# Optimization experiments

Measured on AMD Instinct MI355X. Metric: run time of the kernel, lower is better.

The kernel has to match this reference:

```python
import jax, jax.numpy as jnp
import numpy as np

N, P, D = 8, 4096, 3


def _chamfer_one_direction(x, y, x_lengths, y_lengths):
    # x: (N,P1,D), y: (N,P2,D); squared-L2 k=1 NN of each x point in y (norm=2 in knn_points)
    P1 = x.shape[1]
    P2 = y.shape[1]
    x2 = jnp.sum(x * x, axis=-1)  # (N,P1)
    y2 = jnp.sum(y * y, axis=-1)  # (N,P2)
    d2 = x2[:, :, None] + y2[:, None, :] - 2.0 * jnp.einsum('npd,nqd->npq', x, y)  # (N,P1,P2)
    # mask padded y points out of the NN search
    y_mask = jnp.arange(P2)[None, :] >= y_lengths[:, None]  # (N,P2) True = padded
    d2 = jnp.where(y_mask[:, None, :], jnp.inf, d2)
    cham = jnp.min(d2, axis=2)  # (N,P1) dist to nearest valid y
    # zero out padded x points
    x_mask = jnp.arange(P1)[None, :] >= x_lengths[:, None]  # (N,P1)
    cham = jnp.where(x_mask, 0.0, cham)
    # point_reduction='mean'
    per_cloud = jnp.sum(cham, axis=1) / jnp.maximum(x_lengths, 1).astype(x.dtype)  # (N,)
    # batch_reduction='mean' (no weights -> divide by N)
    return jnp.sum(per_cloud) / x.shape[0]


def setup_inputs() -> dict:
    key = jax.random.key(0)
    k1, k2, k3, k4 = jax.random.split(key, 4)
    x = jax.random.normal(k1, (N, P, D), dtype=jnp.float32)
    y = jax.random.normal(k2, (N, P, D), dtype=jnp.float32)
    x_lengths = jax.random.randint(k3, (N,), P // 2, P + 1)
    y_lengths = jax.random.randint(k4, (N,), P // 2, P + 1)
    return {"x": x, "y": y, "x_lengths": x_lengths, "y_lengths": y_lengths}


def reference(x, y, x_lengths, y_lengths):
    cham_x = _chamfer_one_direction(x, y, x_lengths, y_lengths)
    cham_y = _chamfer_one_direction(y, x, y_lengths, x_lengths)
    return cham_x + cham_y
```

## Files before the change

kernel.cpp:

```cpp
#include <hip/hip_runtime.h>
#include <hip/hip_bf16.h>
#include <math.h>

constexpr int NB  = 8;
constexpr int PP  = 4096;

constexpr int TPB = 256;
constexpr int XPT = 4;
constexpr int XCH = TPB * XPT;
constexpr int NXC = PP / XCH;
constexpr int NYC = 32;
constexpr int YCH = PP / NYC;
constexpr int GRIDA = 2 * NB * NXC * NYC;

constexpr int NSEG = 16;
constexpr int SEGP = PP / NSEG;
constexpr int NPART = 2 * NB * NSEG;

__global__ __launch_bounds__(TPB, 4) void nn_partial(
    const float* __restrict__ x, const float* __restrict__ y,
    const int* __restrict__ xlen, const int* __restrict__ ylen,
    float* __restrict__ ws)
{
    __shared__ float4 sy[YCH];

    const int bid = (int)blockIdx.x;
    const int yc  = bid & (NYC - 1);
    const int xc  = (bid >> 5) & (NXC - 1);
    const int n   = (bid >> 7) & (NB - 1);
    const int dir = bid >> 10;

    const float* __restrict__ xs = dir ? y : x;
    const float* __restrict__ ys = dir ? x : y;
    const int yl = (dir ? xlen : ylen)[n];
    const int ql = (dir ? ylen : xlen)[n];

    const float* __restrict__ yb = ys + (size_t)n * PP * 3;
    if ((int)threadIdx.x < YCH) {
        const int p   = (int)threadIdx.x;
        const int idx = yc + NYC * p;
        float y0 = yb[idx * 3 + 0];
        float y1 = yb[idx * 3 + 1];
        float y2 = yb[idx * 3 + 2];
        sy[p] = make_float4(-2.f * y0, -2.f * y1, -2.f * y2,
                            fmaf(y0, y0, fmaf(y1, y1, y2 * y2)));
    }

    const int wave  = (int)threadIdx.x >> 6;
    const int lane  = (int)threadIdx.x & 63;
    const int wbase = xc * XCH + wave * (XPT * 64);

    float px0[XPT], px1[XPT], px2[XPT], a[XPT], emin[XPT];
    const float* __restrict__ xb = xs + (size_t)n * PP * 3;
#pragma unroll
    for (int k = 0; k < XPT; ++k) {
        const int xi = wbase + k * 64 + lane;
        px0[k] = xb[xi * 3 + 0];
        px1[k] = xb[xi * 3 + 1];
        px2[k] = xb[xi * 3 + 2];
        a[k]   = fmaf(px0[k], px0[k], fmaf(px1[k], px1[k], px2[k] * px2[k]));
        emin[k] = INFINITY;
    }
    __syncthreads();

    int jend = (yl - yc + NYC - 1) >> 5;
    if (jend > YCH) jend = YCH;

    if (ql > wbase && jend > 0) {
        const int j2 = jend & ~1;
#pragma unroll 2
        for (int j = 0; j < j2; j += 2) {
            const float4 u = sy[j];
            const float4 v = sy[j + 1];
#pragma unroll
            for (int k = 0; k < XPT; ++k) {
                float e1 = fmaf(px0[k], u.x, fmaf(px1[k], u.y, fmaf(px2[k], u.z, u.w)));
                float e2 = fmaf(px0[k], v.x, fmaf(px1[k], v.y, fmaf(px2[k], v.z, v.w)));
                emin[k] = fminf(emin[k], fminf(e1, e2));
            }
        }
        if (jend & 1) {
            const float4 u = sy[jend - 1];
#pragma unroll
            for (int k = 0; k < XPT; ++k) {
                float e1 = fmaf(px0[k], u.x, fmaf(px1[k], u.y, fmaf(px2[k], u.z, u.w)));
                emin[k] = fminf(emin[k], e1);
            }
        }
    }

    float* __restrict__ w = ws + ((size_t)(dir * NB + n) * NYC + yc) * PP;
#pragma unroll
    for (int k = 0; k < XPT; ++k) {
        w[wbase + k * 64 + lane] = a[k] + emin[k];
    }
}

__global__ __launch_bounds__(256) void reduce_cloud(
    const float* __restrict__ ws,
    const int* __restrict__ xlen, const int* __restrict__ ylen,
    float* __restrict__ partial)
{
    const int b   = blockIdx.x;
    const int seg = b & (NSEG - 1);
    const int c   = b >> 4;
    const int dir = c >> 3;
    const int n   = c & (NB - 1);
    const int xl  = (dir ? ylen : xlen)[n];

    const float* __restrict__ w = ws + (size_t)c * NYC * PP;
    const int i = seg * SEGP + (int)threadIdx.x;

    float m = w[i];
#pragma unroll
    for (int ch = 1; ch < NYC; ++ch) m = fminf(m, w[(size_t)ch * PP + i]);
    float sum = (i < xl) ? m : 0.f;

#pragma unroll
    for (int off = 32; off > 0; off >>= 1) sum += __shfl_xor(sum, off);
    __shared__ float ls[4];
    const int lane = (int)threadIdx.x & 63;
    const int wv   = (int)threadIdx.x >> 6;
    if (lane == 0) ls[wv] = sum;
    __syncthreads();
    if (threadIdx.x == 0) {
        float tot = ls[0] + ls[1] + ls[2] + ls[3];
        int d = xl > 1 ? xl : 1;
        partial[b] = tot / (float)d / (float)NB;
    }
}

__global__ __launch_bounds__(256) void final_sum(
    const float* __restrict__ partial, float* __restrict__ out)
{
    float v = partial[threadIdx.x];
#pragma unroll
    for (int off = 32; off > 0; off >>= 1) v += __shfl_xor(v, off);
    __shared__ float ls[4];
    const int lane = (int)threadIdx.x & 63;
    const int wv   = (int)threadIdx.x >> 6;
    if (lane == 0) ls[wv] = v;
    __syncthreads();
    if (threadIdx.x == 0) out[0] = ls[0] + ls[1] + ls[2] + ls[3];
}

__global__ __launch_bounds__(TPB) void chamfer_atomic(
    const float* __restrict__ x, const float* __restrict__ y,
    const int* __restrict__ xlen, const int* __restrict__ ylen,
    float* __restrict__ out)
{
    __shared__ float4 sy[YCH];

    int bid = blockIdx.x;
    const int xc  = bid & (NXC - 1); bid >>= 2;
    const int n   = bid & (NB - 1);  bid >>= 3;
    const int dir = bid;

    const float* __restrict__ xs = dir ? y : x;
    const float* __restrict__ ys = dir ? x : y;
    const int yl = (dir ? xlen : ylen)[n];
    const int xl = (dir ? ylen : xlen)[n];

    float m0[XPT], m1[XPT], m2[XPT], a[XPT], emin[XPT];
    const int xi0 = xc * XCH + (int)threadIdx.x;
    const float* __restrict__ xb = xs + (size_t)n * PP * 3;
#pragma unroll
    for (int k = 0; k < XPT; ++k) {
        int xi = xi0 + k * TPB;
        float x0 = xb[xi * 3 + 0];
        float x1 = xb[xi * 3 + 1];
        float x2 = xb[xi * 3 + 2];
        m0[k] = -2.f * x0; m1[k] = -2.f * x1; m2[k] = -2.f * x2;
        a[k]  = fmaf(x0, x0, fmaf(x1, x1, x2 * x2));
        emin[k] = INFINITY;
    }

    for (int yc = 0; yc < NYC; ++yc) {
        const float* __restrict__ ybase = ys + ((size_t)n * PP + (size_t)yc * YCH) * 3;
        __syncthreads();
        if ((int)threadIdx.x < YCH) {
            int p = (int)threadIdx.x;
            float y0 = ybase[p * 3 + 0];
            float y1 = ybase[p * 3 + 1];
            float y2 = ybase[p * 3 + 2];
            sy[p] = make_float4(y0, y1, y2, fmaf(y0, y0, fmaf(y1, y1, y2 * y2)));
        }
        __syncthreads();
        int jend = yl - yc * YCH;
        if (jend > YCH) jend = YCH;
#pragma unroll 4
        for (int j = 0; j < jend; ++j) {
            float4 v = sy[j];
#pragma unroll
            for (int k = 0; k < XPT; ++k) {
                float e = fmaf(m0[k], v.x, fmaf(m1[k], v.y, fmaf(m2[k], v.z, v.w)));
                emin[k] = fminf(emin[k], e);
            }
        }
    }

    float sum = 0.f;
#pragma unroll
    for (int k = 0; k < XPT; ++k) {
        int xi = xi0 + k * TPB;
        if (xi < xl) sum += a[k] + emin[k];
    }
#pragma unroll
    for (int off = 32; off > 0; off >>= 1) sum += __shfl_xor(sum, off);
    __shared__ float ls[4];
    const int lane = (int)threadIdx.x & 63;
    const int wv   = (int)threadIdx.x >> 6;
    if (lane == 0) ls[wv] = sum;
    __syncthreads();
    if (threadIdx.x == 0) {
        float tot = ls[0] + ls[1] + ls[2] + ls[3];
        int d = xl > 1 ? xl : 1;
        atomicAdd(out, tot / (float)d / (float)NB);
    }
}

extern "C" void kernel_launch(void* const* d_in, const int* in_sizes, int n_in,
                              void* d_out, int out_size, void* d_ws, size_t ws_size,
                              hipStream_t stream) {
    const float* x  = (const float*)d_in[0];
    const float* y  = (const float*)d_in[1];
    const int* xl   = (const int*)d_in[2];
    const int* yl   = (const int*)d_in[3];
    float* out      = (float*)d_out;

    const size_t ws_floats = (size_t)2 * NB * NYC * PP;
    const size_t ws_need   = (ws_floats + NPART) * sizeof(float);

    if (ws_size >= ws_need) {
        float* ws      = (float*)d_ws;
        float* partial = ws + ws_floats;
        nn_partial<<<GRIDA, TPB, 0, stream>>>(x, y, xl, yl, ws);
        reduce_cloud<<<NPART, 256, 0, stream>>>(ws, xl, yl, partial);
        final_sum<<<1, 256, 0, stream>>>(partial, out);
    } else {
        hipMemsetAsync(d_out, 0, sizeof(float), stream);
        const int gridF = 2 * NB * NXC;
        chamfer_atomic<<<gridF, TPB, 0, stream>>>(x, y, xl, yl, out);
    }
}
```

Measured before the change: 27.55 us.

## Double x points per thread and split each y slice into two halves

Each thread now holds 8 query points instead of 4, so every shared-memory y load feeds more FMAs. Each y slice is split into two 64-point halves handled by separate blocks, which keeps the grid size the same while halving per-block inner-loop length. The cost is twice as many partial-min rows in the workspace, making the reduction read 64 rows per point instead of 32, plus higher register pressure. The fallback atomic kernel is rewritten to use the same layout and strided y indexing.

```diff
diff --git a/kernel.cpp b/kernel.cpp
--- a/kernel.cpp
+++ b/kernel.cpp
@@ -6,12 +6,14 @@
 constexpr int PP  = 4096;
 
 constexpr int TPB = 256;
-constexpr int XPT = 4;
+constexpr int XPT = 8;
 constexpr int XCH = TPB * XPT;
 constexpr int NXC = PP / XCH;
 constexpr int NYC = 32;
-constexpr int YCH = PP / NYC;
-constexpr int GRIDA = 2 * NB * NXC * NYC;
+constexpr int JH  = 2;
+constexpr int JCH = 64;
+constexpr int NCH = NYC * JH;
+constexpr int GRIDA = 2 * NB * NXC * NYC * JH;
 
 constexpr int NSEG = 16;
 constexpr int SEGP = PP / NSEG;
@@ -22,11 +24,12 @@
     const int* __restrict__ xlen, const int* __restrict__ ylen,
     float* __restrict__ ws)
 {
-    __shared__ float4 sy[YCH];
+    __shared__ float4 sy[JCH];
 
     const int bid = (int)blockIdx.x;
-    const int yc  = bid & (NYC - 1);
-    const int xc  = (bid >> 5) & (NXC - 1);
+    const int jh  = bid & (JH - 1);
+    const int yc  = (bid >> 1) & (NYC - 1);
+    const int xc  = (bid >> 6) & (NXC - 1);
     const int n   = (bid >> 7) & (NB - 1);
     const int dir = bid >> 10;
 
@@ -36,9 +39,9 @@
     const int ql = (dir ? ylen : xlen)[n];
 
     const float* __restrict__ yb = ys + (size_t)n * PP * 3;
-    if ((int)threadIdx.x < YCH) {
+    if ((int)threadIdx.x < JCH) {
         const int p   = (int)threadIdx.x;
-        const int idx = yc + NYC * p;
+        const int idx = yc + NYC * (jh * JCH + p);
         float y0 = yb[idx * 3 + 0];
         float y1 = yb[idx * 3 + 1];
         float y2 = yb[idx * 3 + 2];
@@ -63,11 +66,12 @@
     }
     __syncthreads();
 
-    int jend = (yl - yc + NYC - 1) >> 5;
-    if (jend > YCH) jend = YCH;
-
-    if (ql > wbase && jend > 0) {
-        const int j2 = jend & ~1;
+    int jslice = (yl - yc + NYC - 1) >> 5;
+    int jcnt = jslice - jh * JCH;
+    if (jcnt > JCH) jcnt = JCH;
+
+    if (ql > wbase && jcnt > 0) {
+        const int j2 = jcnt & ~1;
 #pragma unroll 2
         for (int j = 0; j < j2; j += 2) {
             const float4 u = sy[j];
@@ -79,8 +83,8 @@
                 emin[k] = fminf(emin[k], fminf(e1, e2));
             }
         }
-        if (jend & 1) {
-            const float4 u = sy[jend - 1];
+        if (jcnt & 1) {
+            const float4 u = sy[jcnt - 1];
 #pragma unroll
             for (int k = 0; k < XPT; ++k) {
                 float e1 = fmaf(px0[k], u.x, fmaf(px1[k], u.y, fmaf(px2[k], u.z, u.w)));
@@ -89,7 +93,7 @@
         }
     }
 
-    float* __restrict__ w = ws + ((size_t)(dir * NB + n) * NYC + yc) * PP;
+    float* __restrict__ w = ws + ((size_t)(dir * NB + n) * NCH + (yc * JH + jh)) * PP;
 #pragma unroll
     for (int k = 0; k < XPT; ++k) {
         w[wbase + k * 64 + lane] = a[k] + emin[k];
@@ -108,12 +112,12 @@
     const int n   = c & (NB - 1);
     const int xl  = (dir ? ylen : xlen)[n];
 
-    const float* __restrict__ w = ws + (size_t)c * NYC * PP;
+    const float* __restrict__ w = ws + (size_t)c * NCH * PP;
     const int i = seg * SEGP + (int)threadIdx.x;
 
     float m = w[i];
 #pragma unroll
-    for (int ch = 1; ch < NYC; ++ch) m = fminf(m, w[(size_t)ch * PP + i]);
+    for (int ch = 1; ch < NCH; ++ch) m = fminf(m, w[(size_t)ch * PP + i]);
     float sum = (i < xl) ? m : 0.f;
 
 #pragma unroll
@@ -149,51 +153,55 @@
     const int* __restrict__ xlen, const int* __restrict__ ylen,
     float* __restrict__ out)
 {
-    __shared__ float4 sy[YCH];
+    __shared__ float4 sy[JCH];
 
     int bid = blockIdx.x;
-    const int xc  = bid & (NXC - 1); bid >>= 2;
-    const int n   = bid & (NB - 1);  bid >>= 3;
-    const int dir = bid;
+    const int xc  = bid & (NXC - 1);
+    const int n   = (bid >> 1) & (NB - 1);
+    const int dir = bid >> 4;
 
     const float* __restrict__ xs = dir ? y : x;
     const float* __restrict__ ys = dir ? x : y;
     const int yl = (dir ? xlen : ylen)[n];
     const int xl = (dir ? ylen : xlen)[n];
 
-    float m0[XPT], m1[XPT], m2[XPT], a[XPT], emin[XPT];
-    const int xi0 = xc * XCH + (int)threadIdx.x;
+    float px0[XPT], px1[XPT], px2[XPT], a[XPT], emin[XPT];
+    const int wave  = (int)threadIdx.x >> 6;
+    const int lane  = (int)threadIdx.x & 63;
+    const int wbase = xc * XCH + wave * (XPT * 64);
     const float* __restrict__ xb = xs + (size_t)n * PP * 3;
 #pragma unroll
     for (int k = 0; k < XPT; ++k) {
-        int xi = xi0 + k * TPB;
-        float x0 = xb[xi * 3 + 0];
-        float x1 = xb[xi * 3 + 1];
-        float x2 = xb[xi * 3 + 2];
-        m0[k] = -2.f * x0; m1[k] = -2.f * x1; m2[k] = -2.f * x2;
-        a[k]  = fmaf(x0, x0, fmaf(x1, x1, x2 * x2));
+        const int xi = wbase + k * 64 + lane;
+        px0[k] = xb[xi * 3 + 0];
+        px1[k] = xb[xi * 3 + 1];
+        px2[k] = xb[xi * 3 + 2];
+        a[k]   = fmaf(px0[k], px0[k], fmaf(px1[k], px1[k], px2[k] * px2[k]));
         emin[k] = INFINITY;
     }
 
-    for (int yc = 0; yc < NYC; ++yc) {
-        const float* __restrict__ ybase = ys + ((size_t)n * PP + (size_t)yc * YCH) * 3;
+    const float* __restrict__ yb = ys + (size_t)n * PP * 3;
+    for (int half = 0; half < NYC * JH; ++half) {
+        const int yc = half >> 1, jh = half & 1;
         __syncthreads();
-        if ((int)threadIdx.x < YCH) {
-            int p = (int)threadIdx.x;
-            float y0 = ybase[p * 3 + 0];
-            float y1 = ybase[p * 3 + 1];
-            float y2 = ybase[p * 3 + 2];
-            sy[p] = make_float4(y0, y1, y2, fmaf(y0, y0, fmaf(y1, y1, y2 * y2)));
+        if ((int)threadIdx.x < JCH) {
+            const int p   = (int)threadIdx.x;
+            const int idx = yc + NYC * (jh * JCH + p);
+            float y0 = yb[idx * 3 + 0];
+            float y1 = yb[idx * 3 + 1];
+            float y2 = yb[idx * 3 + 2];
+            sy[p] = make_float4(-2.f * y0, -2.f * y1, -2.f * y2,
+                                fmaf(y0, y0, fmaf(y1, y1, y2 * y2)));
         }
         __syncthreads();
-        int jend = yl - yc * YCH;
-        if (jend > YCH) jend = YCH;
-#pragma unroll 4
-        for (int j = 0; j < jend; ++j) {
-            float4 v = sy[j];
+        int jslice = (yl - yc + NYC - 1) >> 5;
+        int jcnt = jslice - jh * JCH;
+        if (jcnt > JCH) jcnt = JCH;
+        for (int j = 0; j < jcnt; ++j) {
+            const float4 u = sy[j];
 #pragma unroll
             for (int k = 0; k < XPT; ++k) {
-                float e = fmaf(m0[k], v.x, fmaf(m1[k], v.y, fmaf(m2[k], v.z, v.w)));
+                float e = fmaf(px0[k], u.x, fmaf(px1[k], u.y, fmaf(px2[k], u.z, u.w)));
                 emin[k] = fminf(emin[k], e);
             }
         }
@@ -202,15 +210,13 @@
     float sum = 0.f;
 #pragma unroll
     for (int k = 0; k < XPT; ++k) {
-        int xi = xi0 + k * TPB;
+        const int xi = wbase + k * 64 + lane;
         if (xi < xl) sum += a[k] + emin[k];
     }
 #pragma unroll
     for (int off = 32; off > 0; off >>= 1) sum += __shfl_xor(sum, off);
     __shared__ float ls[4];
-    const int lane = (int)threadIdx.x & 63;
-    const int wv   = (int)threadIdx.x >> 6;
-    if (lane == 0) ls[wv] = sum;
+    if (lane == 0) ls[wave] = sum;
     __syncthreads();
     if (threadIdx.x == 0) {
         float tot = ls[0] + ls[1] + ls[2] + ls[3];
@@ -228,7 +234,7 @@
     const int* yl   = (const int*)d_in[3];
     float* out      = (float*)d_out;
 
-    const size_t ws_floats = (size_t)2 * NB * NYC * PP;
+    const size_t ws_floats = (size_t)2 * NB * NCH * PP;
     const size_t ws_need   = (ws_floats + NPART) * sizeof(float);
 
     if (ws_size >= ws_need) {
```

Result: slower. 33.26 us (+20.7%).

## Read y points directly from global memory instead of staging in LDS

Applied to the files above, without the earlier changes.

Drops the shared-memory staging of y chunks and the block barrier in both kernels. Each thread now streams y coordinates from global memory with wave-uniform addresses, recomputes |y|^2 per point, and folds the -2 factor into the x registers. The y chunk becomes a contiguous block rather than a strided interleave, and the nn_partial occupancy hint rises from 4 to 8 blocks per CU. This removes LDS traffic and sync but adds one extra FMA chain per y point and depends on scalar or cached loads keeping up.

```diff
diff --git a/kernel.cpp b/kernel.cpp
--- a/kernel.cpp
+++ b/kernel.cpp
@@ -17,13 +17,11 @@
 constexpr int SEGP = PP / NSEG;
 constexpr int NPART = 2 * NB * NSEG;
 
-__global__ __launch_bounds__(TPB, 4) void nn_partial(
+__global__ __launch_bounds__(TPB, 8) void nn_partial(
     const float* __restrict__ x, const float* __restrict__ y,
     const int* __restrict__ xlen, const int* __restrict__ ylen,
     float* __restrict__ ws)
 {
-    __shared__ float4 sy[YCH];
-
     const int bid = (int)blockIdx.x;
     const int yc  = bid & (NYC - 1);
     const int xc  = (bid >> 5) & (NXC - 1);
@@ -35,56 +33,38 @@
     const int yl = (dir ? xlen : ylen)[n];
     const int ql = (dir ? ylen : xlen)[n];
 
-    const float* __restrict__ yb = ys + (size_t)n * PP * 3;
-    if ((int)threadIdx.x < YCH) {
-        const int p   = (int)threadIdx.x;
-        const int idx = yc + NYC * p;
-        float y0 = yb[idx * 3 + 0];
-        float y1 = yb[idx * 3 + 1];
-        float y2 = yb[idx * 3 + 2];
-        sy[p] = make_float4(-2.f * y0, -2.f * y1, -2.f * y2,
-                            fmaf(y0, y0, fmaf(y1, y1, y2 * y2)));
-    }
-
     const int wave  = (int)threadIdx.x >> 6;
     const int lane  = (int)threadIdx.x & 63;
     const int wbase = xc * XCH + wave * (XPT * 64);
 
-    float px0[XPT], px1[XPT], px2[XPT], a[XPT], emin[XPT];
+    float m0[XPT], m1[XPT], m2[XPT], a[XPT], emin[XPT];
     const float* __restrict__ xb = xs + (size_t)n * PP * 3;
 #pragma unroll
     for (int k = 0; k < XPT; ++k) {
         const int xi = wbase + k * 64 + lane;
-        px0[k] = xb[xi * 3 + 0];
-        px1[k] = xb[xi * 3 + 1];
-        px2[k] = xb[xi * 3 + 2];
-        a[k]   = fmaf(px0[k], px0[k], fmaf(px1[k], px1[k], px2[k] * px2[k]));
+        float x0 = xb[xi * 3 + 0];
+        float x1 = xb[xi * 3 + 1];
+        float x2 = xb[xi * 3 + 2];
+        m0[k] = -2.f * x0; m1[k] = -2.f * x1; m2[k] = -2.f * x2;
+        a[k]  = fmaf(x0, x0, fmaf(x1, x1, x2 * x2));
         emin[k] = INFINITY;
     }
-    __syncthreads();
-
-    int jend = (yl - yc + NYC - 1) >> 5;
+
+    int jend = yl - yc * YCH;
     if (jend > YCH) jend = YCH;
 
     if (ql > wbase && jend > 0) {
-        const int j2 = jend & ~1;
-#pragma unroll 2
-        for (int j = 0; j < j2; j += 2) {
-            const float4 u = sy[j];
-            const float4 v = sy[j + 1];
+        const float* __restrict__ yp = ys + ((size_t)n * PP + (size_t)yc * YCH) * 3;
+#pragma unroll 4
+        for (int j = 0; j < jend; ++j) {
+            const float y0 = yp[j * 3 + 0];
+            const float y1 = yp[j * 3 + 1];
+            const float y2 = yp[j * 3 + 2];
+            const float yy = fmaf(y0, y0, fmaf(y1, y1, y2 * y2));
 #pragma unroll
             for (int k = 0; k < XPT; ++k) {
-                float e1 = fmaf(px0[k], u.x, fmaf(px1[k], u.y, fmaf(px2[k], u.z, u.w)));
-                float e2 = fmaf(px0[k], v.x, fmaf(px1[k], v.y, fmaf(px2[k], v.z, v.w)));
-                emin[k] = fminf(emin[k], fminf(e1, e2));
-            }
-        }
-        if (jend & 1) {
-            const float4 u = sy[jend - 1];
-#pragma unroll
-            for (int k = 0; k < XPT; ++k) {
-                float e1 = fmaf(px0[k], u.x, fmaf(px1[k], u.y, fmaf(px2[k], u.z, u.w)));
-                emin[k] = fminf(emin[k], e1);
+                float e = fmaf(m0[k], y0, fmaf(m1[k], y1, fmaf(m2[k], y2, yy)));
+                emin[k] = fminf(emin[k], e);
             }
         }
     }
@@ -149,12 +129,10 @@
     const int* __restrict__ xlen, const int* __restrict__ ylen,
     float* __restrict__ out)
 {
-    __shared__ float4 sy[YCH];
-
     int bid = blockIdx.x;
-    const int xc  = bid & (NXC - 1); bid >>= 2;
-    const int n   = bid & (NB - 1);  bid >>= 3;
-    const int dir = bid;
+    const int xc  = bid & (NXC - 1);
+    const int n   = (bid >> 2) & (NB - 1);
+    const int dir = bid >> 5;
 
     const float* __restrict__ xs = dir ? y : x;
     const float* __restrict__ ys = dir ? x : y;
@@ -162,11 +140,13 @@
     const int xl = (dir ? ylen : xlen)[n];
 
     float m0[XPT], m1[XPT], m2[XPT], a[XPT], emin[XPT];
-    const int xi0 = xc * XCH + (int)threadIdx.x;
+    const int wave  = (int)threadIdx.x >> 6;
+    const int lane  = (int)threadIdx.x & 63;
+    const int wbase = xc * XCH + wave * (XPT * 64);
     const float* __restrict__ xb = xs + (size_t)n * PP * 3;
 #pragma unroll
     for (int k = 0; k < XPT; ++k) {
-        int xi = xi0 + k * TPB;
+        const int xi = wbase + k * 64 + lane;
         float x0 = xb[xi * 3 + 0];
         float x1 = xb[xi * 3 + 1];
         float x2 = xb[xi * 3 + 2];
@@ -175,42 +155,30 @@
         emin[k] = INFINITY;
     }
 
-    for (int yc = 0; yc < NYC; ++yc) {
-        const float* __restrict__ ybase = ys + ((size_t)n * PP + (size_t)yc * YCH) * 3;
-        __syncthreads();
-        if ((int)threadIdx.x < YCH) {
-            int p = (int)threadIdx.x;
-            float y0 = ybase[p * 3 + 0];
-            float y1 = ybase[p * 3 + 1];
-            float y2 = ybase[p * 3 + 2];
-            sy[p] = make_float4(y0, y1, y2, fmaf(y0, y0, fmaf(y1, y1, y2 * y2)));
+    const float* __restrict__ yp = ys + (size_t)n * PP * 3;
+#pragma unroll 4
+    for (int j = 0; j < yl; ++j) {
+        const float y0 = yp[j * 3 + 0];
+        const float y1 = yp[j * 3 + 1];
+        const float y2 = yp[j * 3 + 2];
+        const float yy = fmaf(y0, y0, fmaf(y1, y1, y2 * y2));
+#pragma unroll
+        for (int k = 0; k < XPT; ++k) {
+            float e = fmaf(m0[k], y0, fmaf(m1[k], y1, fmaf(m2[k], y2, yy)));
+            emin[k] = fminf(emin[k], e);
         }
-        __syncthreads();
-        int jend = yl - yc * YCH;
-        if (jend > YCH) jend = YCH;
-#pragma unroll 4
-        for (int j = 0; j < jend; ++j) {
-            float4 v = sy[j];
-#pragma unroll
-            for (int k = 0; k < XPT; ++k) {
-                float e = fmaf(m0[k], v.x, fmaf(m1[k], v.y, fmaf(m2[k], v.z, v.w)));
-                emin[k] = fminf(emin[k], e);
-            }
-        }
     }
 
     float sum = 0.f;
 #pragma unroll
     for (int k = 0; k < XPT; ++k) {
-        int xi = xi0 + k * TPB;
+        const int xi = wbase + k * 64 + lane;
         if (xi < xl) sum += a[k] + emin[k];
     }
 #pragma unroll
     for (int off = 32; off > 0; off >>= 1) sum += __shfl_xor(sum, off);
     __shared__ float ls[4];
-    const int lane = (int)threadIdx.x & 63;
-    const int wv   = (int)threadIdx.x >> 6;
-    if (lane == 0) ls[wv] = sum;
+    if (lane == 0) ls[wave] = sum;
     __syncthreads();
     if (threadIdx.x == 0) {
         float tot = ls[0] + ls[1] + ls[2] + ls[3];
```

Result: slower. 44.15 us (+60.3%).
